# Kernel optimization log

Measured on AMD Instinct MI355X. Metric: run time of the kernel, lower is better.

Reference implementation:

```python
import jax, jax.numpy as jnp
import numpy as np

N_NODES = 50000
N_EDGES = 640000
D_FEAT = 128
NUM_RELS = 8
EPS = 0.0  # init_eps=0, learn_eps=False -> constant buffer


def setup_inputs() -> dict:
    key = jax.random.key(0)
    k_feat, k_w, k_et, k_src, k_dst = jax.random.split(key, 5)
    feat = jax.random.normal(k_feat, (N_NODES, D_FEAT), dtype=jnp.float32)
    # TypedLinear weight: one [in_feat, out_feat] matrix per relation
    W = jax.random.normal(k_w, (NUM_RELS, D_FEAT, D_FEAT), dtype=jnp.float32) * 0.05
    etypes = jax.random.randint(k_et, (N_EDGES,), 0, NUM_RELS, dtype=jnp.int32)
    src = jax.random.randint(k_src, (N_EDGES,), 0, N_NODES, dtype=jnp.int32)
    dst = jax.random.randint(k_dst, (N_EDGES,), 0, N_NODES, dtype=jnp.int32)
    return {"feat": feat, "W": W, "etypes": etypes, "src": src, "dst": dst}


def reference(feat, W, etypes, src, dst):
    # feat: [N, d]; W: [R, d, d]; etypes/src/dst: [E]
    n_nodes = feat.shape[0]
    num_rels = W.shape[0]
    x = feat[src]  # gather source features, [E, d]
    # TypedLinear: m_e = x_e @ W[etype_e]. Loop over the small fixed relation
    # set (grouped-GEMM form) instead of materializing [E, d, d] weights.
    m = jnp.zeros_like(x)
    for r in range(num_rels):
        mask = (etypes == r)[:, None]
        m = m + jnp.where(mask, x, 0.0) @ W[r]
    # sum aggregation over destination nodes (update_all with fn.sum)
    neigh = jax.ops.segment_sum(m, dst, num_segments=n_nodes)  # [N, d]
    # GIN update: (1 + eps) * h + sum of messages; apply_func/activation are None
    return (1.0 + EPS) * feat + neigh
```

## Files before the change

### kernel.cpp

```cpp
#include <hip/hip_runtime.h>
#include <hip/hip_bf16.h>
#include <stdint.h>

#define D 128
#define CAP 48
#define OVFCAP 65536

using bf16x8 = __attribute__((ext_vector_type(8))) short;
using f32x4  = __attribute__((ext_vector_type(4))) float;

__device__ __forceinline__ unsigned short f2bf(float f) {
    unsigned u = __float_as_uint(f);
    u = (u + 0x7fffu + ((u >> 16) & 1u)) >> 16;
    return (unsigned short)u;
}
__device__ __forceinline__ float bf2f(unsigned short h) {
    return __uint_as_float(((unsigned)h) << 16);
}

__device__ __forceinline__ bf16x8 cvt8(float4 a, float4 b) {
    union { bf16x8 v; __hip_bfloat162 h[4]; } u;
    u.h[0] = __float22bfloat162_rn(make_float2(a.x, a.y));
    u.h[1] = __float22bfloat162_rn(make_float2(a.z, a.w));
    u.h[2] = __float22bfloat162_rn(make_float2(b.x, b.y));
    u.h[3] = __float22bfloat162_rn(make_float2(b.z, b.w));
    return u.v;
}

__device__ __forceinline__ uint4 pack2(f32x4 x, f32x4 y) {
    union { uint4 u; __hip_bfloat162 h[4]; } o;
    o.h[0] = __float22bfloat162_rn(make_float2(x[0], x[1]));
    o.h[1] = __float22bfloat162_rn(make_float2(x[2], x[3]));
    o.h[2] = __float22bfloat162_rn(make_float2(y[0], y[1]));
    o.h[3] = __float22bfloat162_rn(make_float2(y[2], y[3]));
    return o.u;
}

__global__ __launch_bounds__(256) void prep3_kernel(
    const float* __restrict__ feat, unsigned short* __restrict__ featb,
    const float* __restrict__ W, unsigned short* __restrict__ Wt,
    int* __restrict__ deg ,
    int N, int fcTotal , int wtTotal)
{
    int zBlocks  = (N + 1 + 255) >> 8;
    int fcBlocks = (fcTotal + 255) >> 8;
    int b = blockIdx.x;
    if (b < zBlocks) {
        int i = b * 256 + threadIdx.x;
        if (i <= N) deg[i] = 0;
    } else if (b < zBlocks + fcBlocks) {
        int i = (b - zBlocks) * 256 + threadIdx.x;
        if (i < fcTotal) {
            const float4* p = (const float4*)feat + (size_t)i * 2;
            *(bf16x8*)(featb + (size_t)i * 8) = cvt8(p[0], p[1]);
        }
    } else {
        int idx = (b - zBlocks - fcBlocks) * 256 + threadIdx.x;
        if (idx < wtTotal) {
            int r = idx >> 14;
            int rem = idx & 16383;
            int k = rem >> 7, c = rem & 127;
            Wt[(r << 14) + (c << 7) + k] = f2bf(W[idx]);
        }
    }
}

__global__ __launch_bounds__(256) void fused3_kernel(
    const unsigned short* __restrict__ featb, const unsigned short* __restrict__ Wt,
    unsigned short* __restrict__ H,
    const int* __restrict__ dst, const int* __restrict__ et,
    const int* __restrict__ src,
    int* __restrict__ deg, unsigned int* __restrict__ slots,
    int* __restrict__ ovf,
    int N, int NBX, int tBlocks, int cntBlocks, int E)
{
    __shared__ __align__(16) unsigned short sW[128 * 128];
    const int b = blockIdx.x;
    const long long total = (long long)tBlocks + cntBlocks;

    long long cb = ((long long)b * cntBlocks) / total;
    bool isCount = (((long long)(b + 1) * cntBlocks) / total) > cb;

    if (isCount) {
        int e = (int)cb * 256 + threadIdx.x;
        if (e < E) {
            int d = dst[e];
            unsigned key = ((unsigned)et[e] * (unsigned)N + (unsigned)src[e]) << 8;
            int ord = atomicAdd(&deg[d], 1);
            if (ord < CAP) {
                slots[(size_t)d * CAP + ord] = key;
            } else {
                int o = atomicAdd(&deg[N], 1);
                if (o < OVFCAP) ovf[o] = e;
            }
        }
        return;
    }

    const int tIdx = b - (int)cb;
    const int rel = tIdx / NBX;
    const int bx  = tIdx - rel * NBX;
    const int tid  = threadIdx.x;
    const int wave = tid >> 6, lane = tid & 63;
    const int q    = lane >> 4, mlo = lane & 15;

    {
        const ulonglong2* wsrc = (const ulonglong2*)(Wt + ((size_t)rel << 14));
        #pragma unroll
        for (int i = 0; i < 8; ++i) {
            int idx = tid + 256 * i;
            int row = idx >> 4, ch = idx & 15;
            ulonglong2 v = wsrc[idx];
            *(ulonglong2*)&sW[row * 128 + ((ch ^ (row & 15)) * 8)] = v;
        }
    }

    const int nb = bx * 128 + wave * 32;
    bf16x8 bfr[2][4];
    int nodeg[2];
    #pragma unroll
    for (int g = 0; g < 2; ++g) {
        int node = nb + g * 16 + mlo;
        nodeg[g] = node;
        int ld = node < N ? node : N - 1;
        const unsigned short* fp = featb + (size_t)ld * D + q * 8;
        #pragma unroll
        for (int ks = 0; ks < 4; ++ks)
            bfr[g][ks] = *(const bf16x8*)(fp + ks * 32);
    }
    __syncthreads();

    const size_t Hb = (size_t)rel * N * D;
    unsigned short* hp0 = H + Hb + (size_t)nodeg[0] * D + q * 8;
    unsigned short* hp1 = H + Hb + (size_t)nodeg[1] * D + q * 8;

    #pragma unroll
    for (int j = 0; j < 4; ++j) {
        bf16x8 af0[4], af1[4];
        const int row0 = (2 * j) * 16 + mlo, row1 = row0 + 16;
        #pragma unroll
        for (int ks = 0; ks < 4; ++ks) {
            af0[ks] = *(const bf16x8*)&sW[row0 * 128 + (((ks * 4 + q) ^ mlo) * 8)];
            af1[ks] = *(const bf16x8*)&sW[row1 * 128 + (((ks * 4 + q) ^ mlo) * 8)];
        }
        #pragma unroll
        for (int g = 0; g < 2; ++g) {
            f32x4 a = {0.f,0.f,0.f,0.f}, c = {0.f,0.f,0.f,0.f};
            #pragma unroll
            for (int ks = 0; ks < 4; ++ks) {
                a = __builtin_amdgcn_mfma_f32_16x16x32_bf16(af0[ks], bfr[g][ks], a, 0, 0, 0);
                c = __builtin_amdgcn_mfma_f32_16x16x32_bf16(af1[ks], bfr[g][ks], c, 0, 0, 0);
            }
            if (nodeg[g] < N)
                *(uint4*)((g ? hp1 : hp0) + j * 32) = pack2(a, c);
        }
    }
}

__global__ __launch_bounds__(256) void k_gather6(
    const char* __restrict__ Hc, const unsigned int* __restrict__ slots,
    const int* __restrict__ deg, const float* __restrict__ feat,
    float* __restrict__ out, int N)
{
    int n = blockIdx.x * 4 + (threadIdx.x >> 6);
    if (n >= N) return;
    int lane = threadIdx.x & 63;
    int h = lane >> 5, l5 = lane & 31;

    float2 acc0 = {0.f, 0.f}, acc1 = {0.f, 0.f};

    int dg = deg[n];
    dg = __builtin_amdgcn_readfirstlane(dg);
    int capped = dg < CAP ? dg : CAP;
    if (capped > 0) {
        unsigned ep = slots[(size_t)n * CAP + (lane < capped ? lane : capped - 1)];
        for (int done = 0; done < capped; done += 32) {
            unsigned long long a[16];
            #pragma unroll
            for (int u = 0; u < 16; ++u) {
                int eidx = done + 2 * u + h;
                int cl = eidx < capped ? eidx : capped - 1;
                unsigned p = __shfl(ep, cl);
                a[u] = *(const unsigned long long*)(Hc + p + l5 * 8);
            }
            #pragma unroll
            for (int u = 0; u < 16; ++u) {
                bool v = (done + 2 * u + h) < capped;
                unsigned lo = (unsigned)a[u], hi = (unsigned)(a[u] >> 32);
                acc0.x += v ? bf2f((unsigned short)(lo & 0xffffu)) : 0.f;
                acc0.y += v ? bf2f((unsigned short)(lo >> 16)) : 0.f;
                acc1.x += v ? bf2f((unsigned short)(hi & 0xffffu)) : 0.f;
                acc1.y += v ? bf2f((unsigned short)(hi >> 16)) : 0.f;
            }
        }
    }
    acc0.x += __shfl(acc0.x, lane ^ 32);
    acc0.y += __shfl(acc0.y, lane ^ 32);
    acc1.x += __shfl(acc1.x, lane ^ 32);
    acc1.y += __shfl(acc1.y, lane ^ 32);
    if (h == 0) {
        int f4 = 8 * (l5 >> 3) + 4 * (l5 & 1) + ((l5 >> 1) & 3);
        float4 fv = ((const float4*)feat)[(size_t)n * 32 + f4];
        float4 o;
        o.x = fv.x + acc0.x; o.y = fv.y + acc0.y;
        o.z = fv.z + acc1.x; o.w = fv.w + acc1.y;
        ((float4*)out)[(size_t)n * 32 + f4] = o;
    }
}

__global__ __launch_bounds__(256) void k_ovf(
    const char* __restrict__ Hc, const int* __restrict__ ovf,
    const int* __restrict__ deg ,
    const int* __restrict__ dst, const int* __restrict__ et,
    const int* __restrict__ src, float* __restrict__ out, int N)
{
    int cnt = deg[N];
    if (cnt > OVFCAP) cnt = OVFCAP;
    int wid = (blockIdx.x * 256 + threadIdx.x) >> 6;
    int nw = (gridDim.x * 256) >> 6;
    int lane = threadIdx.x & 63;
    const int jj = lane >> 4, qq = (lane >> 2) & 3, pp = lane & 3;
    const int f = 16 * jj + 8 * (pp >> 1) + 2 * qq + (pp & 1);
    for (int i = wid; i < cnt; i += nw) {
        int e = ovf[i];
        int d = dst[e];
        unsigned key = ((unsigned)et[e] * (unsigned)N + (unsigned)src[e]) << 8;
        unsigned a = *(const unsigned*)(Hc + key + lane * 4);
        atomicAdd(out + (size_t)d * D + 2 * f,     bf2f((unsigned short)(a & 0xffffu)));
        atomicAdd(out + (size_t)d * D + 2 * f + 1, bf2f((unsigned short)(a >> 16)));
    }
}

__global__ __launch_bounds__(256) void init_kernel(
    const float* __restrict__ feat, float* __restrict__ out, int n4)
{
    int i = blockIdx.x * 256 + threadIdx.x;
    if (i < n4) ((float4*)out)[i] = ((const float4*)feat)[i];
}

__global__ __launch_bounds__(128) void edge_matvec_kernel(
    const float* __restrict__ feat, const float* __restrict__ W,
    const int* __restrict__ et, const int* __restrict__ src,
    const int* __restrict__ dst, float* __restrict__ out, int E)
{
    __shared__ float xs[D];
    int e = blockIdx.x;
    int c = threadIdx.x;
    int s = src[e], r = et[e], d = dst[e];
    xs[c] = feat[(size_t)s * D + c];
    __syncthreads();
    const float* Wr = W + (size_t)r * D * D;
    float acc = 0.f;
    #pragma unroll 8
    for (int k = 0; k < D; ++k) acc += xs[k] * Wr[(size_t)k * D + c];
    atomicAdd(out + (size_t)d * D + c, acc);
}

static inline size_t al256(size_t x) { return (x + 255) & ~(size_t)255; }

extern "C" void kernel_launch(void* const* d_in, const int* in_sizes, int n_in,
                              void* d_out, int out_size, void* d_ws, size_t ws_size,
                              hipStream_t stream) {
    const float* feat = (const float*)d_in[0];
    const float* W    = (const float*)d_in[1];
    const int*   et   = (const int*)d_in[2];
    const int*   src  = (const int*)d_in[3];
    const int*   dst  = (const int*)d_in[4];
    float* out = (float*)d_out;

    const int N = in_sizes[0] / D;
    const int R = in_sizes[1] / (D * D);
    const int E = in_sizes[2];

    size_t hB   = al256((size_t)R * N * D * sizeof(unsigned short));
    size_t wtB  = al256((size_t)R * D * D * sizeof(unsigned short));
    size_t degB = al256((size_t)(N + 1) * sizeof(int));
    size_t sltB = al256((size_t)N * CAP * sizeof(unsigned int));
    size_t ovfB = al256((size_t)OVFCAP * sizeof(int));
    size_t fbB  = al256((size_t)N * D * sizeof(unsigned short));
    size_t need = hB + wtB + degB + sltB + ovfB + fbB;

    const bool packable = ((size_t)R * (size_t)N * 256ull <= 0xFFFFFFFFull);

    if (ws_size >= need && packable) {
        char* p = (char*)d_ws;
        unsigned short* H      = (unsigned short*)p;           p += hB;
        unsigned short* Wt     = (unsigned short*)p;           p += wtB;
        int*            deg    = (int*)p;                      p += degB;
        unsigned int*   slots  = (unsigned int*)p;             p += sltB;
        int*            ovf    = (int*)p;                      p += ovfB;
        unsigned short* featb  = (unsigned short*)p;

        int wtTotal = R * D * D;
        int fcTotal = (N * D) / 8;
        int zBlocks  = (N + 1 + 255) / 256;
        int fcBlocks = (fcTotal + 255) / 256;
        int wtBlocks = (wtTotal + 255) / 256;
        int cntBlocks = (E + 255) / 256;

        prep3_kernel<<<zBlocks + fcBlocks + wtBlocks, 256, 0, stream>>>(
            feat, featb, W, Wt, deg, N, fcTotal, wtTotal);

        int NBX = (N + 127) / 128;
        int tBlocks = NBX * R;
        fused3_kernel<<<tBlocks + cntBlocks, 256, 0, stream>>>(
            featb, Wt, H, dst, et, src, deg, slots, ovf,
            N, NBX, tBlocks, cntBlocks, E);

        k_gather6<<<(N + 3) / 4, 256, 0, stream>>>(
            (const char*)H, slots, deg, feat, out, N);

        k_ovf<<<16, 256, 0, stream>>>(
            (const char*)H, ovf, deg, dst, et, src, out, N);
    } else {
        int n4 = (N * D) / 4;
        init_kernel<<<(n4 + 255) / 256, 256, 0, stream>>>(feat, out, n4);
        edge_matvec_kernel<<<E, 128, 0, stream>>>(feat, W, et, src, dst, out, E);
    }
}
```

Measured before the change: 168.7 us.

## Aggregate raw features per relation before GEMM instead of transforming every node

Swaps the order of transform and aggregation. The old code multiplied every node by all 8 relation matrices into a large bf16 H buffer, then gathered H rows per destination. The new kernel sums bf16 source features per destination into 8 relation buckets and stores them in LDS, then runs one K=1024 MFMA GEMM against the stacked transposed weights and adds feat. This removes the R*N*D intermediate write and read, and the gather now reads featb rows instead of H rows. In exchange, per-edge accumulation uses a divergent switch, partial sums are rounded to bf16 before the GEMM, and overflow edges fall back to a scalar fp32 matvec.

```diff
diff --git a/kernel.cpp b/kernel.cpp
--- a/kernel.cpp
+++ b/kernel.cpp
@@ -5,6 +5,7 @@
 #define D 128
 #define CAP 48
 #define OVFCAP 65536
+#define NPB 32
 
 using bf16x8 = __attribute__((ext_vector_type(8))) short;
 using f32x4  = __attribute__((ext_vector_type(4))) float;
@@ -27,57 +28,23 @@
     return u.v;
 }
 
-__device__ __forceinline__ uint4 pack2(f32x4 x, f32x4 y) {
-    union { uint4 u; __hip_bfloat162 h[4]; } o;
-    o.h[0] = __float22bfloat162_rn(make_float2(x[0], x[1]));
-    o.h[1] = __float22bfloat162_rn(make_float2(x[2], x[3]));
-    o.h[2] = __float22bfloat162_rn(make_float2(y[0], y[1]));
-    o.h[3] = __float22bfloat162_rn(make_float2(y[2], y[3]));
-    return o.u;
-}
-
-__global__ __launch_bounds__(256) void prep3_kernel(
+__global__ __launch_bounds__(256) void k_zero(int* __restrict__ deg, int N)
+{
+    int i = blockIdx.x * 256 + threadIdx.x;
+    if (i <= N) deg[i] = 0;
+}
+
+__global__ __launch_bounds__(256) void prepcnt_kernel(
     const float* __restrict__ feat, unsigned short* __restrict__ featb,
     const float* __restrict__ W, unsigned short* __restrict__ Wt,
-    int* __restrict__ deg ,
-    int N, int fcTotal , int wtTotal)
-{
-    int zBlocks  = (N + 1 + 255) >> 8;
-    int fcBlocks = (fcTotal + 255) >> 8;
-    int b = blockIdx.x;
-    if (b < zBlocks) {
-        int i = b * 256 + threadIdx.x;
-        if (i <= N) deg[i] = 0;
-    } else if (b < zBlocks + fcBlocks) {
-        int i = (b - zBlocks) * 256 + threadIdx.x;
-        if (i < fcTotal) {
-            const float4* p = (const float4*)feat + (size_t)i * 2;
-            *(bf16x8*)(featb + (size_t)i * 8) = cvt8(p[0], p[1]);
-        }
-    } else {
-        int idx = (b - zBlocks - fcBlocks) * 256 + threadIdx.x;
-        if (idx < wtTotal) {
-            int r = idx >> 14;
-            int rem = idx & 16383;
-            int k = rem >> 7, c = rem & 127;
-            Wt[(r << 14) + (c << 7) + k] = f2bf(W[idx]);
-        }
-    }
-}
-
-__global__ __launch_bounds__(256) void fused3_kernel(
-    const unsigned short* __restrict__ featb, const unsigned short* __restrict__ Wt,
-    unsigned short* __restrict__ H,
-    const int* __restrict__ dst, const int* __restrict__ et,
-    const int* __restrict__ src,
+    const int* __restrict__ et, const int* __restrict__ src,
+    const int* __restrict__ dst,
     int* __restrict__ deg, unsigned int* __restrict__ slots,
     int* __restrict__ ovf,
-    int N, int NBX, int tBlocks, int cntBlocks, int E)
-{
-    __shared__ __align__(16) unsigned short sW[128 * 128];
+    int N, int E, int fcTotal, int wtTotal, int fwBlocks, int cntBlocks)
+{
     const int b = blockIdx.x;
-    const long long total = (long long)tBlocks + cntBlocks;
-
+    const long long total = (long long)fwBlocks + cntBlocks;
     long long cb = ((long long)b * cntBlocks) / total;
     bool isCount = (((long long)(b + 1) * cntBlocks) / total) > cb;
 
@@ -85,7 +52,7 @@
         int e = (int)cb * 256 + threadIdx.x;
         if (e < E) {
             int d = dst[e];
-            unsigned key = ((unsigned)et[e] * (unsigned)N + (unsigned)src[e]) << 8;
+            unsigned key = ((unsigned)src[e] << 8) | (unsigned)et[e];
             int ord = atomicAdd(&deg[d], 1);
             if (ord < CAP) {
                 slots[(size_t)d * CAP + ord] = key;
@@ -97,120 +64,150 @@
         return;
     }
 
-    const int tIdx = b - (int)cb;
-    const int rel = tIdx / NBX;
-    const int bx  = tIdx - rel * NBX;
+    int idx = (int)(b - cb);
+    int fcBlocks = (fcTotal + 255) >> 8;
+    if (idx < fcBlocks) {
+        int i = idx * 256 + threadIdx.x;
+        if (i < fcTotal) {
+            const float4* p = (const float4*)feat + (size_t)i * 2;
+            *(bf16x8*)(featb + (size_t)i * 8) = cvt8(p[0], p[1]);
+        }
+    } else {
+        int i2 = (idx - fcBlocks) * 256 + threadIdx.x;
+        if (i2 < wtTotal) {
+            int r = i2 >> 14;
+            int rem = i2 & 16383;
+            int k = rem >> 7, c = rem & 127;
+            Wt[(r << 14) + (c << 7) + k] = f2bf(W[i2]);
+        }
+    }
+}
+
+__global__ __launch_bounds__(256, 2) void gg_kernel(
+    const unsigned short* __restrict__ featb, const unsigned short* __restrict__ Wt,
+    const unsigned int* __restrict__ slots, const int* __restrict__ deg,
+    const float* __restrict__ feat, float* __restrict__ out, int N)
+{
+    __shared__ __align__(16) unsigned short sX[NPB * 1024];
     const int tid  = threadIdx.x;
     const int wave = tid >> 6, lane = tid & 63;
     const int q    = lane >> 4, mlo = lane & 15;
-
-    {
-        const ulonglong2* wsrc = (const ulonglong2*)(Wt + ((size_t)rel << 14));
-        #pragma unroll
-        for (int i = 0; i < 8; ++i) {
-            int idx = tid + 256 * i;
-            int row = idx >> 4, ch = idx & 15;
-            ulonglong2 v = wsrc[idx];
-            *(ulonglong2*)&sW[row * 128 + ((ch ^ (row & 15)) * 8)] = v;
-        }
-    }
-
-    const int nb = bx * 128 + wave * 32;
-    bf16x8 bfr[2][4];
-    int nodeg[2];
+    const int nbase = blockIdx.x * NPB;
+    const int gbase = nbase + wave * 8;
+
+    int dgl;
+    { int nn = gbase + (lane & 7); dgl = (nn < N) ? deg[nn < N ? nn : 0] : 0; }
+
+    const int slotsel = lane < CAP ? lane : CAP - 1;
+    unsigned kv_cur;
+    { int n0 = gbase < N ? gbase : 0; kv_cur = slots[(size_t)n0 * CAP + slotsel]; }
+
+    for (int i = 0; i < 8; ++i) {
+        const int node = gbase + i;
+        int dg = __builtin_amdgcn_readlane(dgl, i);
+        int capped = (node < N) ? (dg < CAP ? dg : CAP) : 0;
+        unsigned kv = kv_cur;
+        if (i < 7) {
+            int n1 = gbase + i + 1; if (n1 >= N) n1 = 0;
+            kv_cur = slots[(size_t)n1 * CAP + slotsel];
+        }
+
+        float acc[16];
+        #pragma unroll
+        for (int r = 0; r < 16; ++r) acc[r] = 0.f;
+
+        for (int done = 0; done < capped; done += 16) {
+            int bc = capped - done; if (bc > 16) bc = 16;
+            unsigned a[16]; unsigned kk[16];
+            #pragma unroll
+            for (int u = 0; u < 16; ++u) if (u < bc) {
+                kk[u] = __builtin_amdgcn_readlane(kv, done + u);
+                a[u] = *(const unsigned*)((const char*)featb
+                         + (size_t)(kk[u] & 0xFFFFFF00u) + (lane << 2));
+            }
+            #pragma unroll
+            for (int u = 0; u < 16; ++u) if (u < bc) {
+                int r = (int)(kk[u] & 0xFFu);
+                float lo = __uint_as_float(a[u] << 16);
+                float hi = __uint_as_float(a[u] & 0xffff0000u);
+                switch (r) {
+                    case 0: acc[0]  += lo; acc[1]  += hi; break;
+                    case 1: acc[2]  += lo; acc[3]  += hi; break;
+                    case 2: acc[4]  += lo; acc[5]  += hi; break;
+                    case 3: acc[6]  += lo; acc[7]  += hi; break;
+                    case 4: acc[8]  += lo; acc[9]  += hi; break;
+                    case 5: acc[10] += lo; acc[11] += hi; break;
+                    case 6: acc[12] += lo; acc[13] += hi; break;
+                    default: acc[14] += lo; acc[15] += hi; break;
+                }
+            }
+        }
+
+        const int slot = wave * 8 + i;
+        char* xb = (char*)sX + (size_t)slot * 2048;
+        const int sw = slot & 15;
+        #pragma unroll
+        for (int r = 0; r < 8; ++r) {
+            __hip_bfloat162 pv = __float22bfloat162_rn(make_float2(acc[2*r], acc[2*r+1]));
+            int chunk = (r << 4) + (lane >> 2);
+            *(unsigned*)(xb + (((chunk ^ sw) << 4) | ((lane & 3) << 2))) = *(unsigned*)&pv;
+        }
+    }
+    __syncthreads();
+
+    const int cbase = wave * 32;
+    f32x4 accm[2][2];
+    #pragma unroll
+    for (int mt = 0; mt < 2; ++mt)
+        #pragma unroll
+        for (int g = 0; g < 2; ++g)
+            accm[mt][g] = (f32x4){0.f, 0.f, 0.f, 0.f};
+
+    const char* xr = (const char*)sX;
+    #pragma unroll 4
+    for (int ks = 0; ks < 32; ++ks) {
+        const int r = ks >> 2;
+        const int joff = ((ks & 3) << 5) + (q << 3);
+        bf16x8 af[2], bfv[2];
+        #pragma unroll
+        for (int mt = 0; mt < 2; ++mt) {
+            int c = cbase + (mt << 4) + mlo;
+            af[mt] = *(const bf16x8*)(Wt + ((size_t)r << 14) + (c << 7) + joff);
+        }
+        #pragma unroll
+        for (int g = 0; g < 2; ++g) {
+            int slot = (g << 4) + mlo;
+            int chunk = (ks << 2) + q;
+            bfv[g] = *(const bf16x8*)(xr + (size_t)slot * 2048
+                        + (((chunk ^ (slot & 15)) << 4)));
+        }
+        #pragma unroll
+        for (int mt = 0; mt < 2; ++mt)
+            #pragma unroll
+            for (int g = 0; g < 2; ++g)
+                accm[mt][g] = __builtin_amdgcn_mfma_f32_16x16x32_bf16(
+                    af[mt], bfv[g], accm[mt][g], 0, 0, 0);
+    }
+
     #pragma unroll
     for (int g = 0; g < 2; ++g) {
-        int node = nb + g * 16 + mlo;
-        nodeg[g] = node;
-        int ld = node < N ? node : N - 1;
-        const unsigned short* fp = featb + (size_t)ld * D + q * 8;
-        #pragma unroll
-        for (int ks = 0; ks < 4; ++ks)
-            bfr[g][ks] = *(const bf16x8*)(fp + ks * 32);
-    }
-    __syncthreads();
-
-    const size_t Hb = (size_t)rel * N * D;
-    unsigned short* hp0 = H + Hb + (size_t)nodeg[0] * D + q * 8;
-    unsigned short* hp1 = H + Hb + (size_t)nodeg[1] * D + q * 8;
-
-    #pragma unroll
-    for (int j = 0; j < 4; ++j) {
-        bf16x8 af0[4], af1[4];
-        const int row0 = (2 * j) * 16 + mlo, row1 = row0 + 16;
-        #pragma unroll
-        for (int ks = 0; ks < 4; ++ks) {
-            af0[ks] = *(const bf16x8*)&sW[row0 * 128 + (((ks * 4 + q) ^ mlo) * 8)];
-            af1[ks] = *(const bf16x8*)&sW[row1 * 128 + (((ks * 4 + q) ^ mlo) * 8)];
-        }
-        #pragma unroll
-        for (int g = 0; g < 2; ++g) {
-            f32x4 a = {0.f,0.f,0.f,0.f}, c = {0.f,0.f,0.f,0.f};
+        int node = nbase + (g << 4) + mlo;
+        if (node < N) {
             #pragma unroll
-            for (int ks = 0; ks < 4; ++ks) {
-                a = __builtin_amdgcn_mfma_f32_16x16x32_bf16(af0[ks], bfr[g][ks], a, 0, 0, 0);
-                c = __builtin_amdgcn_mfma_f32_16x16x32_bf16(af1[ks], bfr[g][ks], c, 0, 0, 0);
+            for (int mt = 0; mt < 2; ++mt) {
+                int c = cbase + (mt << 4) + (q << 2);
+                float4 fv = *(const float4*)(feat + (size_t)node * D + c);
+                f32x4 a = accm[mt][g];
+                float4 o = {fv.x + a[0], fv.y + a[1], fv.z + a[2], fv.w + a[3]};
+                *(float4*)(out + (size_t)node * D + c) = o;
             }
-            if (nodeg[g] < N)
-                *(uint4*)((g ? hp1 : hp0) + j * 32) = pack2(a, c);
-        }
-    }
-}
-
-__global__ __launch_bounds__(256) void k_gather6(
-    const char* __restrict__ Hc, const unsigned int* __restrict__ slots,
-    const int* __restrict__ deg, const float* __restrict__ feat,
-    float* __restrict__ out, int N)
-{
-    int n = blockIdx.x * 4 + (threadIdx.x >> 6);
-    if (n >= N) return;
-    int lane = threadIdx.x & 63;
-    int h = lane >> 5, l5 = lane & 31;
-
-    float2 acc0 = {0.f, 0.f}, acc1 = {0.f, 0.f};
-
-    int dg = deg[n];
-    dg = __builtin_amdgcn_readfirstlane(dg);
-    int capped = dg < CAP ? dg : CAP;
-    if (capped > 0) {
-        unsigned ep = slots[(size_t)n * CAP + (lane < capped ? lane : capped - 1)];
-        for (int done = 0; done < capped; done += 32) {
-            unsigned long long a[16];
-            #pragma unroll
-            for (int u = 0; u < 16; ++u) {
-                int eidx = done + 2 * u + h;
-                int cl = eidx < capped ? eidx : capped - 1;
-                unsigned p = __shfl(ep, cl);
-                a[u] = *(const unsigned long long*)(Hc + p + l5 * 8);
-            }
-            #pragma unroll
-            for (int u = 0; u < 16; ++u) {
-                bool v = (done + 2 * u + h) < capped;
-                unsigned lo = (unsigned)a[u], hi = (unsigned)(a[u] >> 32);
-                acc0.x += v ? bf2f((unsigned short)(lo & 0xffffu)) : 0.f;
-                acc0.y += v ? bf2f((unsigned short)(lo >> 16)) : 0.f;
-                acc1.x += v ? bf2f((unsigned short)(hi & 0xffffu)) : 0.f;
-                acc1.y += v ? bf2f((unsigned short)(hi >> 16)) : 0.f;
-            }
-        }
-    }
-    acc0.x += __shfl(acc0.x, lane ^ 32);
-    acc0.y += __shfl(acc0.y, lane ^ 32);
-    acc1.x += __shfl(acc1.x, lane ^ 32);
-    acc1.y += __shfl(acc1.y, lane ^ 32);
-    if (h == 0) {
-        int f4 = 8 * (l5 >> 3) + 4 * (l5 & 1) + ((l5 >> 1) & 3);
-        float4 fv = ((const float4*)feat)[(size_t)n * 32 + f4];
-        float4 o;
-        o.x = fv.x + acc0.x; o.y = fv.y + acc0.y;
-        o.z = fv.z + acc1.x; o.w = fv.w + acc1.y;
-        ((float4*)out)[(size_t)n * 32 + f4] = o;
-    }
-}
-
-__global__ __launch_bounds__(256) void k_ovf(
-    const char* __restrict__ Hc, const int* __restrict__ ovf,
-    const int* __restrict__ deg ,
+        }
+    }
+}
+
+__global__ __launch_bounds__(256) void k_ovf2(
+    const float* __restrict__ feat, const float* __restrict__ W,
+    const int* __restrict__ ovf, const int* __restrict__ deg,
     const int* __restrict__ dst, const int* __restrict__ et,
     const int* __restrict__ src, float* __restrict__ out, int N)
 {
@@ -219,15 +216,20 @@
     int wid = (blockIdx.x * 256 + threadIdx.x) >> 6;
     int nw = (gridDim.x * 256) >> 6;
     int lane = threadIdx.x & 63;
-    const int jj = lane >> 4, qq = (lane >> 2) & 3, pp = lane & 3;
-    const int f = 16 * jj + 8 * (pp >> 1) + 2 * qq + (pp & 1);
     for (int i = wid; i < cnt; i += nw) {
         int e = ovf[i];
-        int d = dst[e];
-        unsigned key = ((unsigned)et[e] * (unsigned)N + (unsigned)src[e]) << 8;
-        unsigned a = *(const unsigned*)(Hc + key + lane * 4);
-        atomicAdd(out + (size_t)d * D + 2 * f,     bf2f((unsigned short)(a & 0xffffu)));
-        atomicAdd(out + (size_t)d * D + 2 * f + 1, bf2f((unsigned short)(a >> 16)));
+        int d = dst[e], r = et[e], s = src[e];
+        const float* x = feat + (size_t)s * D;
+        const float* Wr = W + (size_t)r * D * D;
+        float a0 = 0.f, a1 = 0.f;
+        #pragma unroll 8
+        for (int k = 0; k < D; ++k) {
+            float xv = x[k];
+            a0 += xv * Wr[(size_t)k * D + 2 * lane];
+            a1 += xv * Wr[(size_t)k * D + 2 * lane + 1];
+        }
+        atomicAdd(out + (size_t)d * D + 2 * lane,     a0);
+        atomicAdd(out + (size_t)d * D + 2 * lane + 1, a1);
     }
 }
 
@@ -272,19 +274,17 @@
     const int R = in_sizes[1] / (D * D);
     const int E = in_sizes[2];
 
-    size_t hB   = al256((size_t)R * N * D * sizeof(unsigned short));
     size_t wtB  = al256((size_t)R * D * D * sizeof(unsigned short));
     size_t degB = al256((size_t)(N + 1) * sizeof(int));
     size_t sltB = al256((size_t)N * CAP * sizeof(unsigned int));
     size_t ovfB = al256((size_t)OVFCAP * sizeof(int));
     size_t fbB  = al256((size_t)N * D * sizeof(unsigned short));
-    size_t need = hB + wtB + degB + sltB + ovfB + fbB;
-
-    const bool packable = ((size_t)R * (size_t)N * 256ull <= 0xFFFFFFFFull);
+    size_t need = wtB + degB + sltB + ovfB + fbB;
+
+    const bool packable = (N <= (1 << 24)) && (R <= 256);
 
     if (ws_size >= need && packable) {
         char* p = (char*)d_ws;
-        unsigned short* H      = (unsigned short*)p;           p += hB;
         unsigned short* Wt     = (unsigned short*)p;           p += wtB;
         int*            deg    = (int*)p;                      p += degB;
         unsigned int*   slots  = (unsigned int*)p;             p += sltB;
@@ -293,25 +293,22 @@
 
         int wtTotal = R * D * D;
         int fcTotal = (N * D) / 8;
-        int zBlocks  = (N + 1 + 255) / 256;
-        int fcBlocks = (fcTotal + 255) / 256;
-        int wtBlocks = (wtTotal + 255) / 256;
-        int cntBlocks = (E + 255) / 256;
-
-        prep3_kernel<<<zBlocks + fcBlocks + wtBlocks, 256, 0, stream>>>(
-            feat, featb, W, Wt, deg, N, fcTotal, wtTotal);
-
-        int NBX = (N + 127) / 128;
-        int tBlocks = NBX * R;
-        fused3_kernel<<<tBlocks + cntBlocks, 256, 0, stream>>>(
-            featb, Wt, H, dst, et, src, deg, slots, ovf,
-            N, NBX, tBlocks, cntBlocks, E);
-
-        k_gather6<<<(N + 3) / 4, 256, 0, stream>>>(
-            (const char*)H, slots, deg, feat, out, N);
-
-        k_ovf<<<16, 256, 0, stream>>>(
-            (const char*)H, ovf, deg, dst, et, src, out, N);
+        int zB  = (N + 1 + 255) / 256;
+        int fcB = (fcTotal + 255) / 256;
+        int wtBk = (wtTotal + 255) / 256;
+        int cntB = (E + 255) / 256;
+        int fwB = fcB + wtBk;
+
+        k_zero<<<zB, 256, 0, stream>>>(deg, N);
+
+        prepcnt_kernel<<<fwB + cntB, 256, 0, stream>>>(
+            feat, featb, W, Wt, et, src, dst, deg, slots, ovf,
+            N, E, fcTotal, wtTotal, fwB, cntB);
+
+        int ggB = (N + NPB - 1) / NPB;
+        gg_kernel<<<ggB, 256, 0, stream>>>(featb, Wt, slots, deg, feat, out, N);
+
+        k_ovf2<<<16, 256, 0, stream>>>(feat, W, ovf, deg, dst, et, src, out, N);
     } else {
         int n4 = (N * D) / 4;
         init_kernel<<<(n4 + 255) / 256, 256, 0, stream>>>(feat, out, n4);
```

Result: slower. 274.2 us (+62.5%).
